# Kernel tuning notes

Measured on AMD Instinct MI355X. Metric: run time of the kernel, lower is better.

The kernel has to match this reference:

```python
import jax, jax.numpy as jnp
import numpy as np

CH = 64  # channels
QK = CH // 8  # query/key projection dim


def setup_inputs() -> dict:
    key = jax.random.key(0)
    ks = jax.random.split(key, 8)
    B, C, H, W = 4, CH, 64, 64
    s = 1.0 / np.sqrt(C)
    x = jax.random.normal(ks[0], (B, C, H, W), dtype=jnp.float32)
    Wq = jax.random.normal(ks[1], (QK, C), dtype=jnp.float32) * s
    bq = jnp.zeros((QK,), dtype=jnp.float32)
    Wk = jax.random.normal(ks[2], (QK, C), dtype=jnp.float32) * s
    bk = jnp.zeros((QK,), dtype=jnp.float32)
    Wv = jax.random.normal(ks[3], (C, C), dtype=jnp.float32) * s
    bv = jnp.zeros((C,), dtype=jnp.float32)
    gamma = jnp.zeros((1,), dtype=jnp.float32)
    return {"x": x, "Wq": Wq, "bq": bq, "Wk": Wk, "bk": bk,
            "Wv": Wv, "bv": bv, "gamma": gamma}


def reference(x, Wq, bq, Wk, bk, Wv, bv, gamma):
    B, C, H, W = x.shape
    # 1x1 convs == per-pixel linear projections over channels
    q = jnp.einsum('bchw,dc->bdhw', x, Wq) + bq[None, :, None, None]
    k = jnp.einsum('bchw,dc->bdhw', x, Wk) + bk[None, :, None, None]
    v = jnp.einsum('bchw,dc->bdhw', x, Wv) + bv[None, :, None, None]
    q = q.reshape(B, -1, H * W)             # [B, QK, HW]
    k = k.reshape(B, -1, H * W)             # [B, QK, HW]
    v = v.reshape(B, C, H * W)              # [B, C, HW]
    # attention[b, i, j] = <q[:, i], k[:, j]>, softmax over j (last dim)
    attn = jax.nn.softmax(jnp.einsum('bdi,bdj->bij', q, k), axis=-1)
    # out = value @ attention^T  -> out[b, c, i] = sum_j v[b,c,j] * attn[b,i,j]
    out = jnp.einsum('bcj,bij->bci', v, attn).reshape(B, C, H, W)
    return gamma[0] * out + x
```

## Files before the change

kernel.cpp:

```cpp
#include <hip/hip_runtime.h>
#include <hip/hip_bf16.h>
#include <stdint.h>

typedef float f32x4 __attribute__((ext_vector_type(4)));
typedef short s16x8 __attribute__((ext_vector_type(8)));
typedef unsigned short u16;
typedef uint8_t u8;

#define LOG2E 1.44269504088896340736f
#define FP8MAX 448.0f

#if __has_builtin(__builtin_amdgcn_exp2f)
#define EXP2F __builtin_amdgcn_exp2f
#else
#define EXP2F exp2f
#endif

__device__ __forceinline__ u16 f2bf(float f) {
    union { float f; uint32_t u; } v; v.f = f;
    uint32_t r = v.u + 0x7FFFu + ((v.u >> 16) & 1u);
    return (u16)(r >> 16);
}
__device__ __forceinline__ uint32_t cvt2bf(float lo, float hi) {
    __hip_bfloat162 h = __float22bfloat162_rn(float2{lo, hi});
    union { __hip_bfloat162 h; uint32_t u; } v; v.h = h; return v.u;
}
__device__ __forceinline__ float bflo2f(uint32_t u) {
    union { uint32_t u; float f; } v; v.u = u << 16; return v.f;
}
__device__ __forceinline__ float bfhi2f(uint32_t u) {
    union { uint32_t u; float f; } v; v.u = u & 0xffff0000u; return v.f;
}
__device__ __forceinline__ uint32_t cvt4fp8(float a, float b, float c, float d) {
    int w = __builtin_amdgcn_cvt_pk_fp8_f32(a, b, 0, false);
    w     = __builtin_amdgcn_cvt_pk_fp8_f32(c, d, w, true);
    return (uint32_t)w;
}
__device__ __forceinline__ void ds_write16(u8* d, uint4 v) {
    uint2 lo; lo.x = v.x; lo.y = v.y;
    uint2 hi; hi.x = v.z; hi.y = v.w;
    *(uint2*)(d)     = lo;
    *(uint2*)(d + 8) = hi;
}
__device__ __forceinline__ void lds_barrier() {
    asm volatile("s_waitcnt lgkmcnt(0)\n\ts_barrier" ::: "memory");
}

__global__ __launch_bounds__(256) void qkv_kernel(
    const float* __restrict__ x,
    const float* __restrict__ Wq, const float* __restrict__ bq,
    const float* __restrict__ Wk, const float* __restrict__ bk,
    const float* __restrict__ Wv, const float* __restrict__ bv,
    u16* __restrict__ QT, u16* __restrict__ KT, u8* __restrict__ Vg)
{
    const int tid  = threadIdx.x;
    const int lane = tid & 63;
    const int wave = tid >> 6;
    const int blk  = blockIdx.x;
    const int b    = blk / 320;
    const int sub  = blk - b * 320;
    const int jt   = sub / 5;
    const int cg   = sub - jt * 5;
    const int j    = (jt << 6) + lane;

    const float* xb = x + (size_t)b * 64 * 4096 + j;
    float xv[64];
#pragma unroll
    for (int c = 0; c < 64; ++c) xv[c] = xb[(size_t)c * 4096];

    if (cg < 4) {
#pragma unroll
        for (int co = 0; co < 4; ++co) {
            const int row = __builtin_amdgcn_readfirstlane(cg * 16 + wave * 4 + co);
            const float* wrow = Wv + row * 64;
            float acc = bv[row];
#pragma unroll
            for (int cin = 0; cin < 64; ++cin) acc += wrow[cin] * xv[cin];
            acc = fminf(fmaxf(acc, -FP8MAX), FP8MAX);
            Vg[((size_t)(b * 64 + row)) * 4096 + j] =
                (u8)(__builtin_amdgcn_cvt_pk_fp8_f32(acc, acc, 0, false) & 0xff);
        }
    } else {
        const bool isQ = (wave < 2);
        const float* Wqk = isQ ? Wq : Wk;
        const float* bqk = isQ ? bq : bk;
        const float scl  = isQ ? LOG2E : 1.0f;
        u16* dst = isQ ? QT : KT;
        const int w2 = wave & 1;
#pragma unroll
        for (int co = 0; co < 4; ++co) {
            const int d = __builtin_amdgcn_readfirstlane(w2 * 4 + co);
            const float* wrow = Wqk + d * 64;
            float acc = bqk[d];
#pragma unroll
            for (int cin = 0; cin < 64; ++cin) acc += wrow[cin] * xv[cin];
            dst[((size_t)b * 4096 + j) * 8 + d] = f2bf(acc * scl);
        }
    }
}

#define VROW 72
#define OXW 65

__global__ __launch_bounds__(1024, 4) void attn_kernel(
    const u16* __restrict__ QT, const u16* __restrict__ KT,
    const u8* __restrict__ Vg, const float* __restrict__ x,
    const float* __restrict__ gamma, float* __restrict__ out)
{
    __shared__ alignas(16) u8 vbuf[4][2][64 * VROW];
    __shared__ uint32_t OxP[12][8 * OXW];
    __shared__ float    Lx[12 * 16];

    const int tid  = threadIdx.x;
    const int lane = tid & 63;
    const int wave = tid >> 6;
    const int col  = lane & 15;
    const int quad = lane >> 4;
    const int qg   = wave & 3;
    const int sp   = wave >> 2;
    const int blk  = blockIdx.x;
    const int b    = blk >> 6;
    const int i0   = (blk & 63) << 6;
    const int iw   = i0 + qg * 16;

    const u16* KTb = KT + (size_t)b * 4096 * 8;
    const u8*  Vb  = Vg + (size_t)b * 64 * 4096;

    const s16x8 z8 = {0,0,0,0,0,0,0,0};
    const f32x4 zero = {0.f, 0.f, 0.f, 0.f};

    const int pcol = ((col & 12) << 1) + (col & 3);

    s16x8 aq = z8;
    if (quad == 0)
        aq = *(const s16x8*)(QT + ((size_t)b * 4096 + iw + col) * 8);

    f32x4 o[4];
#pragma unroll
    for (int nt = 0; nt < 4; ++nt) o[nt] = zero;
    float lsum = 0.f;

    const int srow = (qg << 4) + (lane >> 2);
    const int schk = lane & 3;
    const u8* vsrc = Vb + (size_t)srow * 4096 + schk * 16;
    u8* vdst0 = &vbuf[sp][0][srow * VROW + schk * 16];
    u8* vdst1 = &vbuf[sp][1][srow * VROW + schk * 16];

    const int jbeg = sp << 10;

    s16x8 kb[4];
#pragma unroll
    for (int nt = 0; nt < 4; ++nt) {
        s16x8 kn = z8;
        if (quad == 0)
            kn = *(const s16x8*)(KTb +
                (size_t)(jbeg + ((nt >> 1) << 5) + ((nt & 1) << 2) + pcol) * 8);
        kb[nt] = kn;
    }
    ds_write16(vdst0, *(const uint4*)(vsrc + jbeg));

#pragma unroll 2
    for (int t = 0; t < 16; ++t) {
        const int j0 = jbeg + (t << 6);

        uint4 vstg;
        if (t < 15) vstg = *(const uint4*)(vsrc + j0 + 64);

        f32x4 s[4];
#pragma unroll
        for (int nt = 0; nt < 4; ++nt)
            s[nt] = __builtin_amdgcn_mfma_f32_16x16x32_bf16(kb[nt], aq, zero, 0, 0, 0);

        if (t < 15) {
#pragma unroll
            for (int nt = 0; nt < 4; ++nt) {
                s16x8 kn = z8;
                if (quad == 0)
                    kn = *(const s16x8*)(KTb +
                        (size_t)(j0 + 64 + ((nt >> 1) << 5) + ((nt & 1) << 2) + pcol) * 8);
                kb[nt] = kn;
            }
        }

        uint32_t w[4];
#pragma unroll
        for (int nt = 0; nt < 4; ++nt) {
            float p0 = fminf(EXP2F(s[nt][0]), FP8MAX);
            float p1 = fminf(EXP2F(s[nt][1]), FP8MAX);
            float p2 = fminf(EXP2F(s[nt][2]), FP8MAX);
            float p3 = fminf(EXP2F(s[nt][3]), FP8MAX);
            lsum += (p0 + p1) + (p2 + p3);
            w[nt] = cvt4fp8(p0, p1, p2, p3);
        }
        const long long ap0 = (long long)(((uint64_t)w[1] << 32) | w[0]);
        const long long ap1 = (long long)(((uint64_t)w[3] << 32) | w[2]);

        lds_barrier();

        {
            const u8* vt = &vbuf[sp][t & 1][0];
#pragma unroll
            for (int nt = 0; nt < 4; ++nt) {
                long long b0 = *(const long long*)(vt + (nt * 16 + col) * VROW + quad * 8);
                long long b1 = *(const long long*)(vt + (nt * 16 + col) * VROW + quad * 8 + 32);
                o[nt] = __builtin_amdgcn_mfma_f32_16x16x32_fp8_fp8(ap0, b0, o[nt], 0, 0, 0);
                o[nt] = __builtin_amdgcn_mfma_f32_16x16x32_fp8_fp8(ap1, b1, o[nt], 0, 0, 0);
            }
        }

        if (t < 15) ds_write16((t & 1) ? vdst0 : vdst1, vstg);
    }

    lsum += __shfl_xor(lsum, 16, 64);
    lsum += __shfl_xor(lsum, 32, 64);

    if (sp > 0) {
        const int slice = (sp - 1) * 4 + qg;
        uint32_t* ox = &OxP[slice][0];
#pragma unroll
        for (int nt = 0; nt < 4; ++nt) {
#pragma unroll
            for (int rp = 0; rp < 2; ++rp)
                ox[(quad * 2 + rp) * OXW + nt * 16 + col] =
                    cvt2bf(o[nt][2 * rp], o[nt][2 * rp + 1]);
        }
        if (quad == 0) Lx[slice * 16 + col] = lsum;
    }
    __syncthreads();
    if (sp == 0) {
        float ltot = lsum;
#pragma unroll
        for (int s = 0; s < 3; ++s)
            ltot += Lx[(s * 4 + qg) * 16 + col];
        float linv[4];
#pragma unroll
        for (int r = 0; r < 4; ++r)
            linv[r] = 1.0f / __shfl(ltot, quad * 4 + r, 16);

#pragma unroll
        for (int s = 0; s < 3; ++s) {
            const uint32_t* ox = &OxP[s * 4 + qg][0];
#pragma unroll
            for (int nt = 0; nt < 4; ++nt) {
#pragma unroll
                for (int rp = 0; rp < 2; ++rp) {
                    uint32_t u = ox[(quad * 2 + rp) * OXW + nt * 16 + col];
                    o[nt][2 * rp]     += bflo2f(u);
                    o[nt][2 * rp + 1] += bfhi2f(u);
                }
            }
        }
        const float g = gamma[0];
#pragma unroll
        for (int nt = 0; nt < 4; ++nt) {
            const int c = nt * 16 + col;
#pragma unroll
            for (int r = 0; r < 4; ++r) {
                const int i = iw + quad * 4 + r;
                const size_t idx = ((size_t)(b * 64 + c)) * 4096 + i;
                out[idx] = g * (o[nt][r] * linv[r]) + x[idx];
            }
        }
    }
}

extern "C" void kernel_launch(void* const* d_in, const int* in_sizes, int n_in,
                              void* d_out, int out_size, void* d_ws, size_t ws_size,
                              hipStream_t stream)
{
    const float* x     = (const float*)d_in[0];
    const float* Wq    = (const float*)d_in[1];
    const float* bq    = (const float*)d_in[2];
    const float* Wk    = (const float*)d_in[3];
    const float* bk    = (const float*)d_in[4];
    const float* Wv    = (const float*)d_in[5];
    const float* bv    = (const float*)d_in[6];
    const float* gamma = (const float*)d_in[7];

    u16* QT = (u16*)d_ws;
    u16* KT = QT + (size_t)4 * 4096 * 8;
    u8*  Vg = (u8*)(KT + (size_t)4 * 4096 * 8);

    qkv_kernel<<<1280, 256, 0, stream>>>(x, Wq, bq, Wk, bk, Wv, bv, QT, KT, Vg);
    attn_kernel<<<256, 1024, 0, stream>>>(QT, KT, Vg, x, gamma, (float*)d_out);
}
```

Measured before the change: 96.91 us.

## Double the V staging tile to 128 keys per barrier in attention loop

Each loop iteration now stages 128 keys of V (two 64-byte chunks per row, row stride widened to 144 bytes) instead of 64, halving the number of LDS barriers and loop trips while processing two 64-key sub-steps per iteration. The split 8-byte LDS writes are replaced with direct 16-byte stores. It doubles the LDS used by V buffers and raises register pressure from two staged global loads, which may affect occupancy at 1024 threads.

```diff
diff --git a/kernel.cpp b/kernel.cpp
--- a/kernel.cpp
+++ b/kernel.cpp
@@ -35,12 +35,6 @@
     int w = __builtin_amdgcn_cvt_pk_fp8_f32(a, b, 0, false);
     w     = __builtin_amdgcn_cvt_pk_fp8_f32(c, d, w, true);
     return (uint32_t)w;
-}
-__device__ __forceinline__ void ds_write16(u8* d, uint4 v) {
-    uint2 lo; lo.x = v.x; lo.y = v.y;
-    uint2 hi; hi.x = v.z; hi.y = v.w;
-    *(uint2*)(d)     = lo;
-    *(uint2*)(d + 8) = hi;
 }
 __device__ __forceinline__ void lds_barrier() {
     asm volatile("s_waitcnt lgkmcnt(0)\n\ts_barrier" ::: "memory");
@@ -99,7 +93,7 @@
     }
 }
 
-#define VROW 72
+#define VROW 144
 #define OXW 65
 
 __global__ __launch_bounds__(1024, 4) void attn_kernel(
@@ -140,11 +134,12 @@
     for (int nt = 0; nt < 4; ++nt) o[nt] = zero;
     float lsum = 0.f;
 
-    const int srow = (qg << 4) + (lane >> 2);
-    const int schk = lane & 3;
-    const u8* vsrc = Vb + (size_t)srow * 4096 + schk * 16;
-    u8* vdst0 = &vbuf[sp][0][srow * VROW + schk * 16];
-    u8* vdst1 = &vbuf[sp][1][srow * VROW + schk * 16];
+    const int slot = (qg << 6) + lane;
+    const int srow = slot >> 2;
+    const int c2   = slot & 3;
+    const u8* vsrc = Vb + (size_t)srow * 4096 + c2 * 16;
+    u8* vdst0 = &vbuf[sp][0][srow * VROW + c2 * 16];
+    u8* vdst1 = &vbuf[sp][1][srow * VROW + c2 * 16];
 
     const int jbeg = sp << 10;
 
@@ -157,58 +152,94 @@
                 (size_t)(jbeg + ((nt >> 1) << 5) + ((nt & 1) << 2) + pcol) * 8);
         kb[nt] = kn;
     }
-    ds_write16(vdst0, *(const uint4*)(vsrc + jbeg));
+    *(uint4*)(vdst0)      = *(const uint4*)(vsrc + jbeg);
+    *(uint4*)(vdst0 + 64) = *(const uint4*)(vsrc + jbeg + 64);
 
 #pragma unroll 2
-    for (int t = 0; t < 16; ++t) {
-        const int j0 = jbeg + (t << 6);
-
-        uint4 vstg;
-        if (t < 15) vstg = *(const uint4*)(vsrc + j0 + 64);
-
-        f32x4 s[4];
+    for (int t = 0; t < 8; ++t) {
+        const int j0 = jbeg + (t << 7);
+        const u8* vt = &vbuf[sp][t & 1][0];
+
+        uint4 vstg0, vstg1;
+        if (t < 7) {
+            vstg0 = *(const uint4*)(vsrc + j0 + 128);
+            vstg1 = *(const uint4*)(vsrc + j0 + 192);
+        }
+
+        long long ap0, ap1;
+        uint32_t w[4];
+        f32x4 sv[4];
+
 #pragma unroll
         for (int nt = 0; nt < 4; ++nt)
-            s[nt] = __builtin_amdgcn_mfma_f32_16x16x32_bf16(kb[nt], aq, zero, 0, 0, 0);
-
-        if (t < 15) {
+            sv[nt] = __builtin_amdgcn_mfma_f32_16x16x32_bf16(kb[nt], aq, zero, 0, 0, 0);
+#pragma unroll
+        for (int nt = 0; nt < 4; ++nt) {
+            s16x8 kn = z8;
+            if (quad == 0)
+                kn = *(const s16x8*)(KTb +
+                    (size_t)(j0 + 64 + ((nt >> 1) << 5) + ((nt & 1) << 2) + pcol) * 8);
+            kb[nt] = kn;
+        }
+#pragma unroll
+        for (int nt = 0; nt < 4; ++nt) {
+            float p0 = fminf(EXP2F(sv[nt][0]), FP8MAX);
+            float p1 = fminf(EXP2F(sv[nt][1]), FP8MAX);
+            float p2 = fminf(EXP2F(sv[nt][2]), FP8MAX);
+            float p3 = fminf(EXP2F(sv[nt][3]), FP8MAX);
+            lsum += (p0 + p1) + (p2 + p3);
+            w[nt] = cvt4fp8(p0, p1, p2, p3);
+        }
+        ap0 = (long long)(((uint64_t)w[1] << 32) | w[0]);
+        ap1 = (long long)(((uint64_t)w[3] << 32) | w[2]);
+
+        lds_barrier();
+
+#pragma unroll
+        for (int nt = 0; nt < 4; ++nt) {
+            long long b0 = *(const long long*)(vt + (nt * 16 + col) * VROW + quad * 8);
+            long long b1 = *(const long long*)(vt + (nt * 16 + col) * VROW + quad * 8 + 32);
+            o[nt] = __builtin_amdgcn_mfma_f32_16x16x32_fp8_fp8(ap0, b0, o[nt], 0, 0, 0);
+            o[nt] = __builtin_amdgcn_mfma_f32_16x16x32_fp8_fp8(ap1, b1, o[nt], 0, 0, 0);
+        }
+
+#pragma unroll
+        for (int nt = 0; nt < 4; ++nt)
+            sv[nt] = __builtin_amdgcn_mfma_f32_16x16x32_bf16(kb[nt], aq, zero, 0, 0, 0);
+        if (t < 7) {
 #pragma unroll
             for (int nt = 0; nt < 4; ++nt) {
                 s16x8 kn = z8;
                 if (quad == 0)
                     kn = *(const s16x8*)(KTb +
-                        (size_t)(j0 + 64 + ((nt >> 1) << 5) + ((nt & 1) << 2) + pcol) * 8);
+                        (size_t)(j0 + 128 + ((nt >> 1) << 5) + ((nt & 1) << 2) + pcol) * 8);
                 kb[nt] = kn;
             }
         }
-
-        uint32_t w[4];
-#pragma unroll
-        for (int nt = 0; nt < 4; ++nt) {
-            float p0 = fminf(EXP2F(s[nt][0]), FP8MAX);
-            float p1 = fminf(EXP2F(s[nt][1]), FP8MAX);
-            float p2 = fminf(EXP2F(s[nt][2]), FP8MAX);
-            float p3 = fminf(EXP2F(s[nt][3]), FP8MAX);
+#pragma unroll
+        for (int nt = 0; nt < 4; ++nt) {
+            float p0 = fminf(EXP2F(sv[nt][0]), FP8MAX);
+            float p1 = fminf(EXP2F(sv[nt][1]), FP8MAX);
+            float p2 = fminf(EXP2F(sv[nt][2]), FP8MAX);
+            float p3 = fminf(EXP2F(sv[nt][3]), FP8MAX);
             lsum += (p0 + p1) + (p2 + p3);
             w[nt] = cvt4fp8(p0, p1, p2, p3);
         }
-        const long long ap0 = (long long)(((uint64_t)w[1] << 32) | w[0]);
-        const long long ap1 = (long long)(((uint64_t)w[3] << 32) | w[2]);
-
-        lds_barrier();
-
-        {
-            const u8* vt = &vbuf[sp][t & 1][0];
-#pragma unroll
-            for (int nt = 0; nt < 4; ++nt) {
-                long long b0 = *(const long long*)(vt + (nt * 16 + col) * VROW + quad * 8);
-                long long b1 = *(const long long*)(vt + (nt * 16 + col) * VROW + quad * 8 + 32);
-                o[nt] = __builtin_amdgcn_mfma_f32_16x16x32_fp8_fp8(ap0, b0, o[nt], 0, 0, 0);
-                o[nt] = __builtin_amdgcn_mfma_f32_16x16x32_fp8_fp8(ap1, b1, o[nt], 0, 0, 0);
-            }
-        }
-
-        if (t < 15) ds_write16((t & 1) ? vdst0 : vdst1, vstg);
+        ap0 = (long long)(((uint64_t)w[1] << 32) | w[0]);
+        ap1 = (long long)(((uint64_t)w[3] << 32) | w[2]);
+#pragma unroll
+        for (int nt = 0; nt < 4; ++nt) {
+            long long b0 = *(const long long*)(vt + (nt * 16 + col) * VROW + 64 + quad * 8);
+            long long b1 = *(const long long*)(vt + (nt * 16 + col) * VROW + 64 + quad * 8 + 32);
+            o[nt] = __builtin_amdgcn_mfma_f32_16x16x32_fp8_fp8(ap0, b0, o[nt], 0, 0, 0);
+            o[nt] = __builtin_amdgcn_mfma_f32_16x16x32_fp8_fp8(ap1, b1, o[nt], 0, 0, 0);
+        }
+
+        if (t < 7) {
+            u8* vd = (t & 1) ? vdst0 : vdst1;
+            *(uint4*)(vd)      = vstg0;
+            *(uint4*)(vd + 64) = vstg1;
+        }
     }
 
     lsum += __shfl_xor(lsum, 16, 64);
```

Measured after the change: 116.8 us. 1.21x slower.
